# Performance work log

Hardware: AMD Instinct MI355X
Metric: run time of the kernel (lower is better)

Reference implementation:

```python
import jax, jax.numpy as jnp
import numpy as np

C = 256
R = 2
HEADS = 8
HEAD_DIM = C // HEADS
SCALE = HEAD_DIM ** -0.5
EPS = 1e-5


def setup_inputs() -> dict:
    key = jax.random.key(0)
    ks = jax.random.split(key, 7)
    x = jax.random.normal(ks[0], (8, C, 64, 64), dtype=jnp.float32)
    # qkv 1x1 conv weight [3C, C], no bias
    w_qkv = jax.random.normal(ks[1], (3 * C, C), dtype=jnp.float32) * (C ** -0.5)
    # depthwise ConvTranspose2d(C, C, k=r, stride=r, groups=C): weight [C, r, r], bias [C]
    w_lp = jax.random.normal(ks[2], (C, R, R), dtype=jnp.float32) * 0.5
    b_lp = jax.random.normal(ks[3], (C,), dtype=jnp.float32) * 0.01
    # GroupNorm(1, C) affine params
    gamma = jnp.ones((C,), dtype=jnp.float32)
    beta = jnp.zeros((C,), dtype=jnp.float32)
    # proj 1x1 conv weight [C, C], no bias
    w_proj = jax.random.normal(ks[4], (C, C), dtype=jnp.float32) * (C ** -0.5)
    return {"x": x, "w_qkv": w_qkv, "w_lp": w_lp, "b_lp": b_lp,
            "gamma": gamma, "beta": beta, "w_proj": w_proj}


def reference(x, w_qkv, w_lp, b_lp, gamma, beta, w_proj):
    # sparse_sampler: AvgPool2d(kernel=1, stride=r) == strided subsampling
    xs = x[:, :, ::R, ::R]                      # [B, C, H, W]
    B, _, H, W = xs.shape
    N = H * W
    # qkv 1x1 conv -> [B, 3C, N] -> [B, heads, 3*head_dim, N]
    qkv = jnp.einsum('oc,bcn->bon', w_qkv, xs.reshape(B, C, N))
    qkv = qkv.reshape(B, HEADS, 3 * HEAD_DIM, N)
    q, k, v = jnp.split(qkv, 3, axis=2)         # each [B, h, d, N]
    # attn[b,h,i,j] = softmax_j( (q^T k)[i,j] * scale )
    attn = jax.nn.softmax(jnp.einsum('bhdi,bhdj->bhij', q, k) * SCALE, axis=-1)
    # out[b,h,d,i] = sum_j v[b,h,d,j] attn[b,h,i,j]
    out = jnp.einsum('bhdj,bhij->bhdi', v, attn).reshape(B, C, H, W)
    # depthwise ConvTranspose2d kernel=r stride=r (non-overlapping): broadcast each
    # pixel into an r x r block weighted by the per-channel kernel, plus bias.
    up = jnp.einsum('bchw,cpq->bchpwq', out, w_lp).reshape(B, C, H * R, W * R)
    up = up + b_lp[None, :, None, None]
    # GroupNorm with 1 group: normalize over (C, H, W) per sample
    mu = jnp.mean(up, axis=(1, 2, 3), keepdims=True)
    var = jnp.var(up, axis=(1, 2, 3), keepdims=True)
    normed = (up - mu) * jax.lax.rsqrt(var + EPS)
    normed = normed * gamma[None, :, None, None] + beta[None, :, None, None]
    # proj 1x1 conv
    Bo, _, Ho, Wo = normed.shape
    y = jnp.einsum('oc,bcn->bon', w_proj, normed.reshape(Bo, C, Ho * Wo))
    return y.reshape(Bo, C, Ho, Wo)
```

## Files before the change

### kernel.cpp

```cpp
#include <hip/hip_runtime.h>
#include <hip/hip_bf16.h>

#define ATT_SCALE_L2E 0.2550322540f

typedef __attribute__((ext_vector_type(8))) short bf16x8;
typedef __attribute__((ext_vector_type(4))) short bf16x4;
typedef __attribute__((ext_vector_type(4))) float f32x4;
typedef __attribute__((ext_vector_type(16))) float f32x16;
typedef __attribute__((ext_vector_type(4))) int i32x4;

#define MFMA16(a, b, c) __builtin_amdgcn_mfma_f32_16x16x32_bf16(a, b, c, 0, 0, 0)
#define MFMA32(a, b, c) __builtin_amdgcn_mfma_f32_32x32x16_bf16(a, b, c, 0, 0, 0)

__device__ inline short f2b(float f) {
    return __builtin_bit_cast(short, __float2bfloat16(f));
}

__device__ inline int cvt_pk(float a, float b) {
    int r;
    asm("v_cvt_pk_bf16_f32 %0, %1, %2" : "=v"(r) : "v"(a), "v"(b));
    return r;
}

__global__ __launch_bounds__(256) void wconv_k(const float* __restrict__ w,
                                               short* __restrict__ wb) {
    int i0 = (blockIdx.x * 256 + threadIdx.x) * 8;
    float4 lo = *(const float4*)(w + i0);
    float4 hi = *(const float4*)(w + i0 + 4);
    bf16x8 o;
    o[0] = f2b(lo.x); o[1] = f2b(lo.y); o[2] = f2b(lo.z); o[3] = f2b(lo.w);
    o[4] = f2b(hi.x); o[5] = f2b(hi.y); o[6] = f2b(hi.z); o[7] = f2b(hi.w);
    *(bf16x8*)(wb + i0) = o;
}

__global__ __launch_bounds__(256) void xt_k(const float* __restrict__ x,
                                            short* __restrict__ xt) {
    int b = blockIdx.y;
    int t = threadIdx.x;
    int n = blockIdx.x * 32 + (t >> 3);
    const float* xb = x + (size_t)b * 1048576 + (n >> 5) * 128 + (n & 31) * 2;
    short* dst = xt + ((size_t)b * 1024 + n) * 256;
#pragma unroll
    for (int it = 0; it < 4; ++it) {
        int c = (t & 7) * 8 + it * 64;
        bf16x8 o;
#pragma unroll
        for (int j = 0; j < 8; ++j) o[j] = f2b(xb[(size_t)(c + j) * 4096]);
        *(bf16x8*)(dst + c) = o;
    }
}

__global__ __launch_bounds__(256) void qkv_k(const short* __restrict__ wb,
                                             const short* __restrict__ xt,
                                             short* __restrict__ qt,
                                             short* __restrict__ ktr,
                                             short* __restrict__ vvr) {
    int b = blockIdx.x;
    int ntile = blockIdx.y * 128;
    int otile = blockIdx.z * 64;
    int t = threadIdx.x;
    int w = t >> 6, l = t & 63, g = l >> 4, li = l & 15;
    int oh = (w & 1) * 32, mh = (w >> 1) * 64;
    int o_base = otile + oh;
    int head = o_base / 96;
    int role = (o_base >> 5) % 3;
    size_t bh = (size_t)b * 8 + head;

    const short* arow = wb + (size_t)o_base * 256;
    const short* brow = xt + ((size_t)b * 1024 + ntile + mh) * 256;

    f32x4 zero = {0.f, 0.f, 0.f, 0.f};
    f32x4 acc[2][4];
#pragma unroll
    for (int og = 0; og < 2; ++og)
#pragma unroll
        for (int mg = 0; mg < 4; ++mg) acc[og][mg] = zero;

#pragma unroll
    for (int kc = 0; kc < 256; kc += 32) {
        bf16x8 af[2], bf_[4];
#pragma unroll
        for (int og = 0; og < 2; ++og)
            af[og] = *(const bf16x8*)(arow + (size_t)(og * 16 + li) * 256 + kc + 8 * g);
#pragma unroll
        for (int mg = 0; mg < 4; ++mg)
            bf_[mg] = *(const bf16x8*)(brow + (size_t)(mg * 16 + li) * 256 + kc + 8 * g);
#pragma unroll
        for (int og = 0; og < 2; ++og)
#pragma unroll
            for (int mg = 0; mg < 4; ++mg)
                acc[og][mg] = MFMA16(af[og], bf_[mg], acc[og][mg]);
    }

    __shared__ short Tl[4][32][64];
    short (*Tw)[64] = Tl[w];
    float sc = (role == 0) ? ATT_SCALE_L2E : 1.f;

#pragma unroll
    for (int og = 0; og < 2; ++og)
#pragma unroll
        for (int mg = 0; mg < 4; ++mg)
#pragma unroll
            for (int r = 0; r < 4; ++r) {
                int op = og * 16 + 4 * g + r;
                int qp = (op >> 3) & 3;
                Tw[op][(mg * 16 + li) ^ (qp << 4)] = f2b(acc[og][mg][r] * sc);
            }
    __syncthreads();

    if (role == 0) {
#pragma unroll
        for (int it = 0; it < 4; ++it) {
            int s = it * 64 + l;
            int dq = (l & 3) * 8;
            int n = s >> 2;
            int q2 = dq >> 3;
            bf16x8 vo;
#pragma unroll
            for (int j = 0; j < 8; ++j)
                vo[j] = Tw[dq + j][n ^ (q2 << 4)];
            *(bf16x8*)(qt + ((size_t)bh * 1024 + ntile + mh + n) * 32 + dq) = vo;
        }
    } else if (role == 1) {
        int base_jb = (ntile + mh) >> 5;
#pragma unroll
        for (int it = 0; it < 4; ++it) {
            int s = it * 64 + l;
            int il2 = s & 31;
            int combo = (s >> 5) & 3;
            int jbr = s >> 7;
            int dq = combo * 8;
            int n_rel = jbr * 32 + il2;
            bf16x8 vo;
#pragma unroll
            for (int j = 0; j < 8; ++j)
                vo[j] = Tw[dq + j][n_rel ^ (combo << 4)];
            *(bf16x8*)(ktr + (size_t)bh * 32768 +
                       (size_t)(base_jb + jbr) * 1024 + combo * 256 + il2 * 8) = vo;
        }
    } else {
        int base_jb = (ntile + mh) >> 5;
#pragma unroll
        for (int it = 0; it < 4; ++it) {
            int s = it * 64 + l;
            int il2 = s & 31;
            int combo = (s >> 5) & 3;
            int jbr = s >> 7;
            int pan = combo >> 1, hi2 = combo & 1;
            int q2 = (il2 >> 3) & 3;
            int bn = jbr * 32 + pan * 16 + 4 * hi2;
            bf16x8 vo;
#pragma unroll
            for (int j = 0; j < 4; ++j) vo[j] = Tw[il2][(bn + j) ^ (q2 << 4)];
#pragma unroll
            for (int j = 0; j < 4; ++j) vo[4 + j] = Tw[il2][(bn + 8 + j) ^ (q2 << 4)];
            *(bf16x8*)(vvr + (size_t)bh * 32768 +
                       (size_t)(base_jb + jbr) * 1024 + combo * 256 + il2 * 8) = vo;
        }
    }
}

__global__ __launch_bounds__(512) void attn_k(const short* __restrict__ qt,
                                              const short* __restrict__ ktr,
                                              const short* __restrict__ vvr,
                                              float* __restrict__ ao2) {
    int bh = blockIdx.x;
    int b = bh >> 3, h = bh & 7;
    int t = threadIdx.x;
    int w = t >> 6, l = t & 63;
    int il = l & 31, hi = l >> 5;
    int wq = w & 3, jh = w >> 2;
    int ibase = blockIdx.y * 128 + wq * 32;

    const short* qtb = qt + (size_t)bh * 32768;
    const short* kbase = ktr + (size_t)bh * 32768 + jh * 16384 + hi * 256 + il * 8;
    const short* vbase = vvr + (size_t)bh * 32768 + jh * 16384 + hi * 256 + il * 8;

    bf16x8 qf0 = *(const bf16x8*)(qtb + (size_t)(ibase + il) * 32 + 8 * hi);
    bf16x8 qf1 = *(const bf16x8*)(qtb + (size_t)(ibase + il) * 32 + 16 + 8 * hi);

    f32x16 zero16 = {0.f,0.f,0.f,0.f,0.f,0.f,0.f,0.f,0.f,0.f,0.f,0.f,0.f,0.f,0.f,0.f};
    f32x16 oacc = zero16;
    float lr0 = 0.f, lr1 = 0.f, lr2 = 0.f, lr3 = 0.f;

#pragma unroll 2
    for (int jb = 0; jb < 16; ++jb) {
        const short* kp = kbase + (size_t)jb * 1024;
        const short* vp = vbase + (size_t)jb * 1024;
        bf16x8 kf0 = *(const bf16x8*)(kp);
        bf16x8 kf1 = *(const bf16x8*)(kp + 512);
        f32x16 s = MFMA32(kf0, qf0, zero16);
        s = MFMA32(kf1, qf1, s);

        float p[16];
#pragma unroll
        for (int r = 0; r < 16; ++r) p[r] = exp2f(s[r]);
        lr0 += p[0] + p[4] + p[8]  + p[12];
        lr1 += p[1] + p[5] + p[9]  + p[13];
        lr2 += p[2] + p[6] + p[10] + p[14];
        lr3 += p[3] + p[7] + p[11] + p[15];

        i32x4 fa, fb;
        fa[0] = cvt_pk(p[0], p[1]);   fa[1] = cvt_pk(p[2], p[3]);
        fa[2] = cvt_pk(p[4], p[5]);   fa[3] = cvt_pk(p[6], p[7]);
        fb[0] = cvt_pk(p[8], p[9]);   fb[1] = cvt_pk(p[10], p[11]);
        fb[2] = cvt_pk(p[12], p[13]); fb[3] = cvt_pk(p[14], p[15]);
        bf16x8 pfa = __builtin_bit_cast(bf16x8, fa);
        bf16x8 pfb = __builtin_bit_cast(bf16x8, fb);

        bf16x8 vfa = *(const bf16x8*)(vp);
        bf16x8 vfb = *(const bf16x8*)(vp + 512);
        oacc = MFMA32(vfa, pfa, oacc);
        oacc = MFMA32(vfb, pfb, oacc);
    }

    float lrun = (lr0 + lr1) + (lr2 + lr3);

    __shared__ float OB[4][64][20];
    __shared__ float LB[4][32];

    if (jh == 1) {
#pragma unroll
        for (int r4 = 0; r4 < 4; ++r4) {
            float4 v = {oacc[r4 * 4], oacc[r4 * 4 + 1], oacc[r4 * 4 + 2], oacc[r4 * 4 + 3]};
            *(float4*)&OB[wq][l][r4 * 4] = v;
        }
        float tu = lrun + __shfl_xor(lrun, 32);
        if (hi == 0) LB[wq][il] = tu;
    }
    __syncthreads();
    if (jh == 0) {
#pragma unroll
        for (int r = 0; r < 16; ++r) oacc[r] += OB[wq][l][r];
        float tl = lrun + __shfl_xor(lrun, 32);
        float inv = 1.f / (tl + LB[wq][il]);

        float* base = ao2 + ((size_t)(b * 256 + h * 32)) * 1024 + ibase + il;
#pragma unroll
        for (int r = 0; r < 16; ++r) {
            int d = (r & 3) + 8 * (r >> 2) + 4 * hi;
            base[(size_t)d * 1024] = oacc[r] * inv;
        }
    }
}

__global__ __launch_bounds__(64) void psum_k(const float* __restrict__ ao2,
                                             float* __restrict__ p1,
                                             float* __restrict__ p2) {
    int row = blockIdx.x;
    const float* base = ao2 + (size_t)row * 1024;
    int l = threadIdx.x;
    float s = 0.f, q = 0.f;
#pragma unroll
    for (int t = 0; t < 4; ++t) {
        float4 v = *(const float4*)(base + l * 4 + t * 256);
        s += v.x + v.y + v.z + v.w;
        q += v.x * v.x + v.y * v.y + v.z * v.z + v.w * v.w;
    }
#pragma unroll
    for (int o = 1; o < 64; o <<= 1) {
        s += __shfl_xor(s, o);
        q += __shfl_xor(q, o);
    }
    if (l == 0) { p1[row] = s; p2[row] = q; }
}

__global__ __launch_bounds__(256) void stats_k(const float* __restrict__ p1,
                                               const float* __restrict__ p2,
                                               const float* __restrict__ wlp,
                                               const float* __restrict__ blp,
                                               float* __restrict__ stats) {
    int b = blockIdx.x, c = threadIdx.x;
    float s = p1[b * 256 + c];
    float q = p2[b * 256 + c];
    float w0 = wlp[c * 4], w1 = wlp[c * 4 + 1], w2 = wlp[c * 4 + 2], w3 = wlp[c * 4 + 3];
    float S1 = w0 + w1 + w2 + w3, S2 = w0 * w0 + w1 * w1 + w2 * w2 + w3 * w3;
    float bl = blp[c];
    float su = S1 * s + 4096.f * bl;
    float sq = S2 * q + 2.f * bl * S1 * s + 4096.f * bl * bl;
    __shared__ float rs_[256], rq_[256];
    rs_[c] = su; rq_[c] = sq;
    __syncthreads();
    for (int o = 128; o > 0; o >>= 1) {
        if (c < o) { rs_[c] += rs_[c + o]; rq_[c] += rq_[c + o]; }
        __syncthreads();
    }
    if (c == 0) {
        const float N = 1048576.f;
        float mu = rs_[0] / N;
        float var = rq_[0] / N - mu * mu;
        stats[b] = mu;
        stats[8 + b] = rsqrtf(var + 1e-5f);
    }
}

__global__ __launch_bounds__(256) void proj_k(const float* __restrict__ ao2,
                                              const float* __restrict__ wp,
                                              const float* __restrict__ wlp,
                                              const float* __restrict__ blp,
                                              const float* __restrict__ gamma,
                                              const float* __restrict__ beta,
                                              const float* __restrict__ stats,
                                              float* __restrict__ y) {
    int b = blockIdx.x;
    int mt = blockIdx.y;
    int otile = blockIdx.z * 64;
    float mu = stats[b], rs = stats[8 + b];

    __shared__ short As[64][40];
    __shared__ short Bs[128][40];

    int t = threadIdx.x;
    int w = t >> 6, l = t & 63, g = l >> 4, li = l & 15;
    int oh = (w >> 1) * 32, mh = (w & 1) * 64;

    f32x4 zero = {0.f, 0.f, 0.f, 0.f};
    f32x4 acc[2][4];
#pragma unroll
    for (int og = 0; og < 2; ++og)
#pragma unroll
        for (int mg = 0; mg < 4; ++mg) acc[og][mg] = zero;

    int so = t >> 2, sc = (t & 3) * 8;
    int bc = t & 31, bm = (t >> 5) * 16;
    int p = t >> 7;
    int wbase = bm & 63;

    for (int kc = 0; kc < 256; kc += 32) {
        const float* wrow = wp + (size_t)(otile + so) * 256 + kc + sc;
#pragma unroll
        for (int j = 0; j < 8; ++j) As[so][sc + j] = f2b(wrow[j]);
        int c = kc + bc;
        float Ac = gamma[c] * rs;
        float Dc = Ac * (blp[c] - mu) + beta[c];
        float w0 = Ac * wlp[c * 4 + p * 2 + 0];
        float w1 = Ac * wlp[c * 4 + p * 2 + 1];
        const float* arow = ao2 + ((size_t)(b * 256 + c)) * 1024 + mt * 32 + (wbase >> 1);
        float4 a0 = *(const float4*)arow;
        float4 a1 = *(const float4*)(arow + 4);
        float av[8] = {a0.x, a0.y, a0.z, a0.w, a1.x, a1.y, a1.z, a1.w};
#pragma unroll
        for (int k = 0; k < 8; ++k) {
            Bs[bm + 2 * k    ][bc] = f2b(w0 * av[k] + Dc);
            Bs[bm + 2 * k + 1][bc] = f2b(w1 * av[k] + Dc);
        }
        __syncthreads();
        bf16x8 af[2], bf_[4];
#pragma unroll
        for (int og = 0; og < 2; ++og) af[og] = *(const bf16x8*)&As[oh + og * 16 + li][8 * g];
#pragma unroll
        for (int mg = 0; mg < 4; ++mg) bf_[mg] = *(const bf16x8*)&Bs[mh + mg * 16 + li][8 * g];
#pragma unroll
        for (int og = 0; og < 2; ++og)
#pragma unroll
            for (int mg = 0; mg < 4; ++mg) acc[og][mg] = MFMA16(af[og], bf_[mg], acc[og][mg]);
        __syncthreads();
    }

#pragma unroll
    for (int og = 0; og < 2; ++og) {
        int o = otile + oh + og * 16 + 4 * g;
#pragma unroll
        for (int mg = 0; mg < 4; ++mg) {
            int m = mt * 128 + mh + mg * 16 + li;
            float* yp = y + ((size_t)b * 256 + o) * 4096 + m;
#pragma unroll
            for (int r = 0; r < 4; ++r) yp[(size_t)r * 4096] = acc[og][mg][r];
        }
    }
}

extern "C" void kernel_launch(void* const* d_in, const int* in_sizes, int n_in,
                              void* d_out, int out_size, void* d_ws, size_t ws_size,
                              hipStream_t stream) {
    const float* x      = (const float*)d_in[0];
    const float* w_qkv  = (const float*)d_in[1];
    const float* w_lp   = (const float*)d_in[2];
    const float* b_lp   = (const float*)d_in[3];
    const float* gamma  = (const float*)d_in[4];
    const float* beta   = (const float*)d_in[5];
    const float* w_proj = (const float*)d_in[6];
    float* y = (float*)d_out;

    short* qt   = (short*)d_out;
    short* ktr  = qt + 2097152;
    short* vvr  = ktr + 2097152;
    short* xt   = vvr + 2097152;
    short* wbuf = xt + 2097152;

    float* ao2   = (float*)d_ws;
    float* p1    = ao2 + 2097152;
    float* p2    = p1 + 2048;
    float* stats = p2 + 2048;

    wconv_k<<<96, 256, 0, stream>>>(w_qkv, wbuf);
    xt_k<<<dim3(32, 8), 256, 0, stream>>>(x, xt);
    qkv_k<<<dim3(8, 8, 12), 256, 0, stream>>>(wbuf, xt, qt, ktr, vvr);
    attn_k<<<dim3(64, 8), 512, 0, stream>>>(qt, ktr, vvr, ao2);
    psum_k<<<2048, 64, 0, stream>>>(ao2, p1, p2);
    stats_k<<<8, 256, 0, stream>>>(p1, p2, w_lp, b_lp, stats);
    proj_k<<<dim3(8, 32, 4), 256, 0, stream>>>(ao2, w_proj, w_lp, b_lp, gamma, beta, stats, y);
}
```

Baseline: 78.68 us.

## Store attention output pixel-major and fold GroupNorm offset into projection bias

The attention output is now written pixel-major ([b][n][c]) with float4 stores instead of channel-major scalar stores. The partial-sum kernel is restructured to read that layout, giving 64 blocks of 256 threads in place of 2048 small blocks. The stats kernel precomputes per-channel scale tables and a per-output constant (W_proj times the normalized bias term). The projection then only multiplies activations by a scale, loads weights straight to registers with packed bf16 conversion, and adds the constant in the epilogue. This is meant to cut strided stores and per-tile normalization arithmetic, at the cost of a longer serial stats kernel with only 8 blocks and a less parallel psum.

```diff
diff --git a/kernel.cpp b/kernel.cpp
--- a/kernel.cpp
+++ b/kernel.cpp
@@ -163,7 +163,7 @@
 __global__ __launch_bounds__(512) void attn_k(const short* __restrict__ qt,
                                               const short* __restrict__ ktr,
                                               const short* __restrict__ vvr,
-                                              float* __restrict__ ao2) {
+                                              float* __restrict__ ao_t) {
     int bh = blockIdx.x;
     int b = bh >> 3, h = bh & 7;
     int t = threadIdx.x;
@@ -235,50 +235,53 @@
         float tl = lrun + __shfl_xor(lrun, 32);
         float inv = 1.f / (tl + LB[wq][il]);
 
-        float* base = ao2 + ((size_t)(b * 256 + h * 32)) * 1024 + ibase + il;
-#pragma unroll
-        for (int r = 0; r < 16; ++r) {
-            int d = (r & 3) + 8 * (r >> 2) + 4 * hi;
-            base[(size_t)d * 1024] = oacc[r] * inv;
-        }
-    }
-}
-
-__global__ __launch_bounds__(64) void psum_k(const float* __restrict__ ao2,
-                                             float* __restrict__ p1,
-                                             float* __restrict__ p2) {
-    int row = blockIdx.x;
-    const float* base = ao2 + (size_t)row * 1024;
-    int l = threadIdx.x;
+        float* basep = ao_t + ((size_t)(b * 1024 + ibase + il)) * 256 + h * 32 + 4 * hi;
+#pragma unroll
+        for (int rr = 0; rr < 4; ++rr) {
+            float4 v = {oacc[rr * 4 + 0] * inv, oacc[rr * 4 + 1] * inv,
+                        oacc[rr * 4 + 2] * inv, oacc[rr * 4 + 3] * inv};
+            *(float4*)(basep + 8 * rr) = v;
+        }
+    }
+}
+
+__global__ __launch_bounds__(256) void psum_k(const float* __restrict__ ao_t,
+                                              float* __restrict__ p1,
+                                              float* __restrict__ p2) {
+    int nc = blockIdx.x, b = blockIdx.y, c = threadIdx.x;
+    const float* base = ao_t + ((size_t)b * 1024 + nc * 128) * 256 + c;
     float s = 0.f, q = 0.f;
-#pragma unroll
-    for (int t = 0; t < 4; ++t) {
-        float4 v = *(const float4*)(base + l * 4 + t * 256);
-        s += v.x + v.y + v.z + v.w;
-        q += v.x * v.x + v.y * v.y + v.z * v.z + v.w * v.w;
-    }
-#pragma unroll
-    for (int o = 1; o < 64; o <<= 1) {
-        s += __shfl_xor(s, o);
-        q += __shfl_xor(q, o);
-    }
-    if (l == 0) { p1[row] = s; p2[row] = q; }
+#pragma unroll 4
+    for (int n = 0; n < 128; ++n) {
+        float v = base[(size_t)n * 256];
+        s += v; q += v * v;
+    }
+    int idx = (b * 8 + nc) * 256 + c;
+    p1[idx] = s; p2[idx] = q;
 }
 
 __global__ __launch_bounds__(256) void stats_k(const float* __restrict__ p1,
                                                const float* __restrict__ p2,
                                                const float* __restrict__ wlp,
                                                const float* __restrict__ blp,
-                                               float* __restrict__ stats) {
+                                               const float* __restrict__ gamma,
+                                               const float* __restrict__ beta,
+                                               const float* __restrict__ wp,
+                                               float* __restrict__ stab,
+                                               float* __restrict__ ktab) {
     int b = blockIdx.x, c = threadIdx.x;
-    float s = p1[b * 256 + c];
-    float q = p2[b * 256 + c];
+    float s = 0.f, q = 0.f;
+    for (int nc = 0; nc < 8; ++nc) {
+        s += p1[(b * 8 + nc) * 256 + c];
+        q += p2[(b * 8 + nc) * 256 + c];
+    }
     float w0 = wlp[c * 4], w1 = wlp[c * 4 + 1], w2 = wlp[c * 4 + 2], w3 = wlp[c * 4 + 3];
     float S1 = w0 + w1 + w2 + w3, S2 = w0 * w0 + w1 * w1 + w2 * w2 + w3 * w3;
     float bl = blp[c];
     float su = S1 * s + 4096.f * bl;
     float sq = S2 * q + 2.f * bl * S1 * s + 4096.f * bl * bl;
     __shared__ float rs_[256], rq_[256];
+    __shared__ float mss[2];
     rs_[c] = su; rq_[c] = sq;
     __syncthreads();
     for (int o = 128; o > 0; o >>= 1) {
@@ -289,31 +292,59 @@
         const float N = 1048576.f;
         float mu = rs_[0] / N;
         float var = rq_[0] / N - mu * mu;
-        stats[b] = mu;
-        stats[8 + b] = rsqrtf(var + 1e-5f);
-    }
-}
-
-__global__ __launch_bounds__(256) void proj_k(const float* __restrict__ ao2,
+        mss[0] = mu;
+        mss[1] = rsqrtf(var + 1e-5f);
+    }
+    __syncthreads();
+    float mu = mss[0], rs = mss[1];
+
+    float Ac = gamma[c] * rs;
+    stab[(b * 4 + 0) * 256 + c] = Ac * w0;
+    stab[(b * 4 + 1) * 256 + c] = Ac * w1;
+    stab[(b * 4 + 2) * 256 + c] = Ac * w2;
+    stab[(b * 4 + 3) * 256 + c] = Ac * w3;
+
+    int o = c;
+    const float* wrow = wp + (size_t)o * 256;
+    float acc = 0.f;
+#pragma unroll 4
+    for (int cc = 0; cc < 256; cc += 4) {
+        float4 wv = *(const float4*)(wrow + cc);
+        float4 gv = *(const float4*)(gamma + cc);
+        float4 lv = *(const float4*)(blp + cc);
+        float4 bv = *(const float4*)(beta + cc);
+        acc += wv.x * (gv.x * rs * (lv.x - mu) + bv.x);
+        acc += wv.y * (gv.y * rs * (lv.y - mu) + bv.y);
+        acc += wv.z * (gv.z * rs * (lv.z - mu) + bv.z);
+        acc += wv.w * (gv.w * rs * (lv.w - mu) + bv.w);
+    }
+    ktab[b * 256 + o] = acc;
+}
+
+__global__ __launch_bounds__(256) void proj_k(const float* __restrict__ ao_t,
                                               const float* __restrict__ wp,
-                                              const float* __restrict__ wlp,
-                                              const float* __restrict__ blp,
-                                              const float* __restrict__ gamma,
-                                              const float* __restrict__ beta,
-                                              const float* __restrict__ stats,
+                                              const float* __restrict__ stab,
+                                              const float* __restrict__ ktab,
                                               float* __restrict__ y) {
     int b = blockIdx.x;
     int mt = blockIdx.y;
     int otile = blockIdx.z * 64;
-    float mu = stats[b], rs = stats[8 + b];
-
-    __shared__ short As[64][40];
-    __shared__ short Bs[128][40];
-
     int t = threadIdx.x;
     int w = t >> 6, l = t & 63, g = l >> 4, li = l & 15;
     int oh = (w >> 1) * 32, mh = (w & 1) * 64;
 
+    __shared__ short Bs[128][40];
+
+    int sm = t >> 1;
+    int sc = (t & 1) * 16;
+    int gm = mt * 128 + sm;
+    int sn = (gm >> 7) * 32 + ((gm & 63) >> 1);
+    int spq = ((gm >> 6) & 1) * 2 + (gm & 1);
+    const float* sao = ao_t + ((size_t)b * 1024 + sn) * 256 + sc;
+    const float* sst = stab + ((size_t)b * 4 + spq) * 256 + sc;
+
+    const float* wrowf = wp + (size_t)(otile + oh) * 256;
+
     f32x4 zero = {0.f, 0.f, 0.f, 0.f};
     f32x4 acc[2][4];
 #pragma unroll
@@ -321,51 +352,50 @@
 #pragma unroll
         for (int mg = 0; mg < 4; ++mg) acc[og][mg] = zero;
 
-    int so = t >> 2, sc = (t & 3) * 8;
-    int bc = t & 31, bm = (t >> 5) * 16;
-    int p = t >> 7;
-    int wbase = bm & 63;
-
     for (int kc = 0; kc < 256; kc += 32) {
-        const float* wrow = wp + (size_t)(otile + so) * 256 + kc + sc;
-#pragma unroll
-        for (int j = 0; j < 8; ++j) As[so][sc + j] = f2b(wrow[j]);
-        int c = kc + bc;
-        float Ac = gamma[c] * rs;
-        float Dc = Ac * (blp[c] - mu) + beta[c];
-        float w0 = Ac * wlp[c * 4 + p * 2 + 0];
-        float w1 = Ac * wlp[c * 4 + p * 2 + 1];
-        const float* arow = ao2 + ((size_t)(b * 256 + c)) * 1024 + mt * 32 + (wbase >> 1);
-        float4 a0 = *(const float4*)arow;
-        float4 a1 = *(const float4*)(arow + 4);
-        float av[8] = {a0.x, a0.y, a0.z, a0.w, a1.x, a1.y, a1.z, a1.w};
-#pragma unroll
-        for (int k = 0; k < 8; ++k) {
-            Bs[bm + 2 * k    ][bc] = f2b(w0 * av[k] + Dc);
-            Bs[bm + 2 * k + 1][bc] = f2b(w1 * av[k] + Dc);
+        int* dst = (int*)&Bs[sm][sc];
+#pragma unroll
+        for (int q4 = 0; q4 < 4; ++q4) {
+            float4 av = *(const float4*)(sao + kc + q4 * 4);
+            float4 sv = *(const float4*)(sst + kc + q4 * 4);
+            dst[q4 * 2 + 0] = cvt_pk(av.x * sv.x, av.y * sv.y);
+            dst[q4 * 2 + 1] = cvt_pk(av.z * sv.z, av.w * sv.w);
+        }
+        bf16x8 af[2];
+#pragma unroll
+        for (int og = 0; og < 2; ++og) {
+            const float* wr = wrowf + (size_t)(og * 16 + li) * 256 + kc + 8 * g;
+            float4 x0 = *(const float4*)(wr);
+            float4 x1 = *(const float4*)(wr + 4);
+            i32x4 aw;
+            aw[0] = cvt_pk(x0.x, x0.y); aw[1] = cvt_pk(x0.z, x0.w);
+            aw[2] = cvt_pk(x1.x, x1.y); aw[3] = cvt_pk(x1.z, x1.w);
+            af[og] = __builtin_bit_cast(bf16x8, aw);
         }
         __syncthreads();
-        bf16x8 af[2], bf_[4];
-#pragma unroll
-        for (int og = 0; og < 2; ++og) af[og] = *(const bf16x8*)&As[oh + og * 16 + li][8 * g];
-#pragma unroll
-        for (int mg = 0; mg < 4; ++mg) bf_[mg] = *(const bf16x8*)&Bs[mh + mg * 16 + li][8 * g];
+        bf16x8 bf_[4];
+#pragma unroll
+        for (int mg = 0; mg < 4; ++mg)
+            bf_[mg] = *(const bf16x8*)&Bs[mh + mg * 16 + li][8 * g];
 #pragma unroll
         for (int og = 0; og < 2; ++og)
 #pragma unroll
-            for (int mg = 0; mg < 4; ++mg) acc[og][mg] = MFMA16(af[og], bf_[mg], acc[og][mg]);
+            for (int mg = 0; mg < 4; ++mg)
+                acc[og][mg] = MFMA16(af[og], bf_[mg], acc[og][mg]);
         __syncthreads();
     }
 
 #pragma unroll
     for (int og = 0; og < 2; ++og) {
-        int o = otile + oh + og * 16 + 4 * g;
-#pragma unroll
-        for (int mg = 0; mg < 4; ++mg) {
-            int m = mt * 128 + mh + mg * 16 + li;
-            float* yp = y + ((size_t)b * 256 + o) * 4096 + m;
-#pragma unroll
-            for (int r = 0; r < 4; ++r) yp[(size_t)r * 4096] = acc[og][mg][r];
+#pragma unroll
+        for (int r = 0; r < 4; ++r) {
+            int o = otile + oh + og * 16 + 4 * g + r;
+            float kv = ktab[b * 256 + o];
+#pragma unroll
+            for (int mg = 0; mg < 4; ++mg) {
+                int m = mt * 128 + mh + mg * 16 + li;
+                y[((size_t)b * 256 + o) * 4096 + m] = acc[og][mg][r] + kv;
+            }
         }
     }
 }
@@ -388,16 +418,17 @@
     short* xt   = vvr + 2097152;
     short* wbuf = xt + 2097152;
 
-    float* ao2   = (float*)d_ws;
-    float* p1    = ao2 + 2097152;
-    float* p2    = p1 + 2048;
-    float* stats = p2 + 2048;
+    float* ao_t  = (float*)d_ws;
+    float* p1    = ao_t + 2097152;
+    float* p2    = p1 + 16384;
+    float* stab  = p2 + 16384;
+    float* ktab  = stab + 8192;
 
     wconv_k<<<96, 256, 0, stream>>>(w_qkv, wbuf);
     xt_k<<<dim3(32, 8), 256, 0, stream>>>(x, xt);
     qkv_k<<<dim3(8, 8, 12), 256, 0, stream>>>(wbuf, xt, qt, ktr, vvr);
-    attn_k<<<dim3(64, 8), 512, 0, stream>>>(qt, ktr, vvr, ao2);
-    psum_k<<<2048, 64, 0, stream>>>(ao2, p1, p2);
-    stats_k<<<8, 256, 0, stream>>>(p1, p2, w_lp, b_lp, stats);
-    proj_k<<<dim3(8, 32, 4), 256, 0, stream>>>(ao2, w_proj, w_lp, b_lp, gamma, beta, stats, y);
-}
+    attn_k<<<dim3(64, 8), 512, 0, stream>>>(qt, ktr, vvr, ao_t);
+    psum_k<<<dim3(8, 8), 256, 0, stream>>>(ao_t, p1, p2);
+    stats_k<<<8, 256, 0, stream>>>(p1, p2, w_lp, b_lp, gamma, beta, w_proj, stab, ktab);
+    proj_k<<<dim3(8, 32, 4), 256, 0, stream>>>(ao_t, w_proj, stab, ktab, y);
+}
```

Measured after the change: 108.9 us. 1.38x slower.
